# Kernel optimization log

Measured on AMD Instinct MI355X. Metric: run time of the kernel, lower is better.

## Reference

```python
import jax, jax.numpy as jnp
import numpy as np

# Config constants (from cfg in init_kwargs)
B = 4            # batch size (num point clouds)
V = 80000        # total pillars across batch
P = 20           # max points per pillar
C_IN = 4         # x, y, z, intensity
C_OUT = 64       # PillarFeatureNet output channels
NY = NX = 640    # BEV grid
BEV_M = 100.0    # bev_range_m per axis
Z_CUT = 5.0
VX = BEV_M / NX              # 0.15625 m
VY = BEV_M / NY
X_OFF = VX / 2.0 - BEV_M / 2.0   # voxel-center offset, pc_range_min + vx/2
Y_OFF = VY / 2.0 - BEV_M / 2.0
BN_EPS = 1e-3


def setup_inputs() -> dict:
    key = jax.random.key(0)
    k1, k2, k3, k4 = jax.random.split(key, 4)
    # points: xy in [-50, 50), z in [-5, 5), intensity in [0, 1)
    xy = jax.random.uniform(k1, (V, P, 2), jnp.float32, -BEV_M / 2, BEV_M / 2)
    z = jax.random.uniform(k2, (V, P, 1), jnp.float32, -Z_CUT, Z_CUT)
    intensity = jax.random.uniform(k3, (V, P, 1), jnp.float32)
    voxels = jnp.concatenate([xy, z, intensity], axis=-1)  # [V, P, 4]
    num_points = jax.random.randint(k4, (V,), 1, P + 1).astype(jnp.int32)
    # unique pillar coordinates (hard voxelization never emits duplicates)
    rng = np.random.default_rng(0)
    flat = rng.choice(B * NY * NX, size=V, replace=False).astype(np.int32)
    b = flat // (NY * NX)
    rem = flat % (NY * NX)
    y = rem // NX
    x = rem % NX
    coors = jnp.asarray(np.stack([b, np.zeros_like(b), y, x], axis=-1))  # [V,4] (b,z,y,x)
    # PFN layer params: Linear(9->64, bias=False) + BN1d(64)
    W = jax.random.normal(jax.random.fold_in(key, 10), (9, C_OUT), jnp.float32) * 0.05
    gamma = jnp.ones((C_OUT,), jnp.float32)
    beta = jnp.zeros((C_OUT,), jnp.float32)
    running_mean = jnp.zeros((C_OUT,), jnp.float32)
    running_var = jnp.ones((C_OUT,), jnp.float32)
    return {"voxels": voxels, "num_points": num_points, "coors": coors,
            "W": W, "gamma": gamma, "beta": beta,
            "running_mean": running_mean, "running_var": running_var}


def reference(voxels, num_points, coors, W, gamma, beta, running_mean, running_var):
    dt = voxels.dtype
    xyz = voxels[..., :3]                                       # [V,P,3]
    npts = jnp.maximum(num_points, 1).astype(dt)[:, None, None]
    # cluster-center offsets (mean over valid points; padded slots are zero here,
    # matching hard voxelization which zero-pads)
    valid = (jnp.arange(P)[None, :] < num_points[:, None])      # [V,P] bool
    xyz_m = xyz * valid[..., None].astype(dt)
    f_cluster = xyz - jnp.sum(xyz_m, axis=1, keepdims=True) / npts
    # voxel-center offsets (xy only, legacy PillarFeatureNet)
    cx = coors[:, 3].astype(dt)[:, None, None] * VX + X_OFF
    cy = coors[:, 2].astype(dt)[:, None, None] * VY + Y_OFF
    f_center = jnp.concatenate([voxels[..., 0:1] - cx, voxels[..., 1:2] - cy], axis=-1)
    feats = jnp.concatenate([voxels, f_cluster, f_center], axis=-1)  # [V,P,9]
    feats = feats * valid[..., None].astype(dt)
    # PFN layer: linear -> BN1d (eval, running stats) -> relu -> max over points
    h = jnp.einsum('vpi,io->vpo', feats, W)                     # [V,P,64]
    h = (h - running_mean) * jax.lax.rsqrt(running_var + BN_EPS) * gamma + beta
    h = jax.nn.relu(h)
    pillar_feats = jnp.max(h, axis=1)                           # [V,64]
    # scatter to dense BEV canvas [B, C, NY, NX]
    flat = coors[:, 0] * (NY * NX) + coors[:, 2] * NX + coors[:, 3]  # [V]
    canvas = jnp.zeros((B * NY * NX, C_OUT), dt).at[flat].set(pillar_feats)
    canvas = canvas.reshape(B, NY, NX, C_OUT).transpose(0, 3, 1, 2)
    occ = jnp.zeros((B * NY * NX, 1), dt).at[flat].set(jnp.ones((V, 1), dt))
    occ = occ.reshape(B, NY, NX, 1).transpose(0, 3, 1, 2)
    return canvas, occ
```

## Files before the change

kernel.cpp:

```cpp
#include <hip/hip_runtime.h>

constexpr int B_    = 4;
constexpr int V_    = 80000;
constexpr int P_    = 20;
constexpr int COUT  = 64;
constexpr int NX_   = 640;
constexpr int NY_   = 640;
constexpr int NYX   = NX_ * NY_;
constexpr float BEV = 100.0f;
constexpr float VXc = BEV / NX_;
constexpr float VYc = BEV / NY_;
constexpr float XOFF = VXc * 0.5f - BEV * 0.5f;
constexpr float YOFF = VYc * 0.5f - BEV * 0.5f;
constexpr float EPS  = 0.001f;

typedef float  vf4 __attribute__((ext_vector_type(4)));

__global__ __launch_bounds__(256) void pillar_feat_kernel(
    const float* __restrict__ voxels,
    const int*   __restrict__ num_points,
    const int*   __restrict__ coors,
    const float* __restrict__ W,
    const float* __restrict__ gamma_,
    const float* __restrict__ beta_,
    const float* __restrict__ rmean,
    const float* __restrict__ rvar,
    float* __restrict__ feat,
    int*   __restrict__ idxmap)
{
    const int v = blockIdx.x * 4 + (threadIdx.x >> 6);
    const int c = threadIdx.x & 63;
    if (v >= V_) return;

    int n = num_points[v];
    n = n < 1 ? 1 : (n > P_ ? P_ : n);

    const int4 co = ((const int4*)coors)[v];
    const int cb = co.x, cyi = co.z, cxi = co.w;

    const float scale = gamma_[c] * rsqrtf(rvar[c] + EPS);
    const float bias  = beta_[c] - rmean[c] * scale;
    float w[9];
    #pragma unroll
    for (int i = 0; i < 9; ++i) w[i] = W[i * COUT + c] * scale;

    const float wcx = w[0] + w[4] + w[7];
    const float wcy = w[1] + w[5] + w[8];
    const float wcz = w[2] + w[6];
    const float wcw = w[3];

    const float4* __restrict__ pv =
        (const float4*)(voxels + (size_t)v * (P_ * 4));

    float sx = 0.f, sy = 0.f, sz = 0.f;
    float dmax = -3.4e38f;
    for (int p = 0; p < n; ++p) {
        float4 q = pv[p];
        sx += q.x; sy += q.y; sz += q.z;
        float d = q.x * wcx + q.y * wcy + q.z * wcz + q.w * wcw;
        dmax = fmaxf(dmax, d);
    }
    const float inv = 1.0f / (float)n;
    const float ccx = (float)cxi * VXc + XOFF;
    const float ccy = (float)cyi * VYc + YOFF;
    const float btot = bias - (sx * inv) * w[4] - (sy * inv) * w[5]
                            - (sz * inv) * w[6] - ccx * w[7] - ccy * w[8];

    float m = dmax + btot;
    if (n < P_) m = fmaxf(m, bias);

    feat[(size_t)v * COUT + c] = fmaxf(m, 0.0f);

    if (c == 0) idxmap[cb * NYX + cyi * NX_ + cxi] = v;
}

__global__ __launch_bounds__(256) void scatter_kernel(
    const float* __restrict__ feat,
    const int*   __restrict__ idxmap,
    const int*   __restrict__ coors,
    float* __restrict__ canvas,
    float* __restrict__ occ)
{
    const int t = blockIdx.x * blockDim.x + threadIdx.x;
    if (t >= (B_ * NYX) / 4) return;

    int4 id = ((const int4*)idxmap)[t];
    const int cell0 = t * 4;
    const int b   = cell0 / NYX;
    const int rem = cell0 - b * NYX;

    const int4* __restrict__ co4 = (const int4*)coors;
    auto check = [&](int idx, int cell) -> int {
        if (idx < 0 || idx >= V_) return -1;
        int4 co = co4[idx];
        return (co.x * NYX + co.z * NX_ + co.w == cell) ? idx : -1;
    };
    id.x = check(id.x, cell0 + 0);
    id.y = check(id.y, cell0 + 1);
    id.z = check(id.z, cell0 + 2);
    id.w = check(id.w, cell0 + 3);

    vf4 o = { id.x >= 0 ? 1.f : 0.f,
              id.y >= 0 ? 1.f : 0.f,
              id.z >= 0 ? 1.f : 0.f,
              id.w >= 0 ? 1.f : 0.f };
    __builtin_nontemporal_store(o, (vf4*)(occ + cell0));

    const float4* __restrict__ f4 = (const float4*)feat;
    const size_t base = (size_t)b * COUT * NYX + (size_t)rem;

    #pragma unroll
    for (int cg = 0; cg < 16; ++cg) {
        float4 a0 = make_float4(0.f, 0.f, 0.f, 0.f);
        float4 a1 = a0, a2 = a0, a3 = a0;
        if (id.x >= 0) a0 = f4[(size_t)id.x * 16 + cg];
        if (id.y >= 0) a1 = f4[(size_t)id.y * 16 + cg];
        if (id.z >= 0) a2 = f4[(size_t)id.z * 16 + cg];
        if (id.w >= 0) a3 = f4[(size_t)id.w * 16 + cg];
        vf4 s0 = { a0.x, a1.x, a2.x, a3.x };
        vf4 s1 = { a0.y, a1.y, a2.y, a3.y };
        vf4 s2 = { a0.z, a1.z, a2.z, a3.z };
        vf4 s3 = { a0.w, a1.w, a2.w, a3.w };
        float* p0 = canvas + base + (size_t)(4 * cg + 0) * NYX;
        __builtin_nontemporal_store(s0, (vf4*)p0);
        __builtin_nontemporal_store(s1, (vf4*)(p0 + NYX));
        __builtin_nontemporal_store(s2, (vf4*)(p0 + 2 * NYX));
        __builtin_nontemporal_store(s3, (vf4*)(p0 + 3 * NYX));
    }
}

extern "C" void kernel_launch(void* const* d_in, const int* in_sizes, int n_in,
                              void* d_out, int out_size, void* d_ws, size_t ws_size,
                              hipStream_t stream) {
    const float* voxels     = (const float*)d_in[0];
    const int*   num_points = (const int*)  d_in[1];
    const int*   coors      = (const int*)  d_in[2];
    const float* W          = (const float*)d_in[3];
    const float* gamma_     = (const float*)d_in[4];
    const float* beta_      = (const float*)d_in[5];
    const float* rmean      = (const float*)d_in[6];
    const float* rvar       = (const float*)d_in[7];

    float* canvas = (float*)d_out;
    float* occ    = (float*)d_out + (size_t)B_ * COUT * NYX;

    float* feat   = (float*)d_ws;
    int*   idxmap = (int*)((char*)d_ws + (size_t)V_ * COUT * sizeof(float));

    pillar_feat_kernel<<<(V_ + 3) / 4, 256, 0, stream>>>(
        voxels, num_points, coors, W, gamma_, beta_, rmean, rvar, feat, idxmap);

    scatter_kernel<<<(B_ * NYX / 4 + 255) / 256, 256, 0, stream>>>(
        feat, idxmap, coors, canvas, occ);
}
```

Measured before the change: 514.4 us.

## Memset idxmap each call, drop coors validation, unroll point loop

The index map is now cleared to -1 with a memset on every launch. That lets the scatter kernel stop re-reading coors to check whether a stale index matches the cell. Empty cells read from a zeroed row in the workspace, so the loads are no longer predicated. The per-pillar point loop is unrolled by four with masking, which may read past n but stays inside the 20-point pillar. The cost is an extra 6.5 MB memset pass in exchange for fewer dependent gathers in scatter.

```diff
diff --git a/kernel.cpp b/kernel.cpp
--- a/kernel.cpp
+++ b/kernel.cpp
@@ -26,10 +26,14 @@
     const float* __restrict__ rmean,
     const float* __restrict__ rvar,
     float* __restrict__ feat,
-    int*   __restrict__ idxmap)
+    int*   __restrict__ idxmap,
+    float* __restrict__ zrow)
 {
     const int v = blockIdx.x * 4 + (threadIdx.x >> 6);
     const int c = threadIdx.x & 63;
+
+    if (blockIdx.x == 0 && threadIdx.x < COUT) zrow[threadIdx.x] = 0.0f;
+
     if (v >= V_) return;
 
     int n = num_points[v];
@@ -54,11 +58,22 @@
 
     float sx = 0.f, sy = 0.f, sz = 0.f;
     float dmax = -3.4e38f;
-    for (int p = 0; p < n; ++p) {
-        float4 q = pv[p];
-        sx += q.x; sy += q.y; sz += q.z;
-        float d = q.x * wcx + q.y * wcy + q.z * wcz + q.w * wcw;
-        dmax = fmaxf(dmax, d);
+    for (int p0 = 0; p0 < n; p0 += 4) {
+        float4 q0 = pv[p0];
+        float4 q1 = pv[p0 + 1];
+        float4 q2 = pv[p0 + 2];
+        float4 q3 = pv[p0 + 3];
+        #pragma unroll
+        for (int j = 0; j < 4; ++j) {
+            float4 q = (j == 0) ? q0 : (j == 1) ? q1 : (j == 2) ? q2 : q3;
+            const bool ok = (p0 + j) < n;
+            const float msk = ok ? 1.0f : 0.0f;
+            sx = fmaf(q.x, msk, sx);
+            sy = fmaf(q.y, msk, sy);
+            sz = fmaf(q.z, msk, sz);
+            float d = fmaf(q.x, wcx, fmaf(q.y, wcy, fmaf(q.z, wcz, q.w * wcw)));
+            dmax = fmaxf(dmax, ok ? d : -3.4e38f);
+        }
     }
     const float inv = 1.0f / (float)n;
     const float ccx = (float)cxi * VXc + XOFF;
@@ -77,28 +92,25 @@
 __global__ __launch_bounds__(256) void scatter_kernel(
     const float* __restrict__ feat,
     const int*   __restrict__ idxmap,
-    const int*   __restrict__ coors,
+    const float* __restrict__ zrow,
     float* __restrict__ canvas,
     float* __restrict__ occ)
 {
     const int t = blockIdx.x * blockDim.x + threadIdx.x;
     if (t >= (B_ * NYX) / 4) return;
 
-    int4 id = ((const int4*)idxmap)[t];
+    const int4 id = ((const int4*)idxmap)[t];
     const int cell0 = t * 4;
     const int b   = cell0 / NYX;
     const int rem = cell0 - b * NYX;
 
-    const int4* __restrict__ co4 = (const int4*)coors;
-    auto check = [&](int idx, int cell) -> int {
-        if (idx < 0 || idx >= V_) return -1;
-        int4 co = co4[idx];
-        return (co.x * NYX + co.z * NX_ + co.w == cell) ? idx : -1;
-    };
-    id.x = check(id.x, cell0 + 0);
-    id.y = check(id.y, cell0 + 1);
-    id.z = check(id.z, cell0 + 2);
-    id.w = check(id.w, cell0 + 3);
+    const float4* __restrict__ f4 = (const float4*)feat;
+    const float4* __restrict__ z4 = (const float4*)zrow;
+
+    const float4* p0r = (id.x >= 0) ? (f4 + (size_t)id.x * 16) : z4;
+    const float4* p1r = (id.y >= 0) ? (f4 + (size_t)id.y * 16) : z4;
+    const float4* p2r = (id.z >= 0) ? (f4 + (size_t)id.z * 16) : z4;
+    const float4* p3r = (id.w >= 0) ? (f4 + (size_t)id.w * 16) : z4;
 
     vf4 o = { id.x >= 0 ? 1.f : 0.f,
               id.y >= 0 ? 1.f : 0.f,
@@ -106,17 +118,14 @@
               id.w >= 0 ? 1.f : 0.f };
     __builtin_nontemporal_store(o, (vf4*)(occ + cell0));
 
-    const float4* __restrict__ f4 = (const float4*)feat;
     const size_t base = (size_t)b * COUT * NYX + (size_t)rem;
 
     #pragma unroll
     for (int cg = 0; cg < 16; ++cg) {
-        float4 a0 = make_float4(0.f, 0.f, 0.f, 0.f);
-        float4 a1 = a0, a2 = a0, a3 = a0;
-        if (id.x >= 0) a0 = f4[(size_t)id.x * 16 + cg];
-        if (id.y >= 0) a1 = f4[(size_t)id.y * 16 + cg];
-        if (id.z >= 0) a2 = f4[(size_t)id.z * 16 + cg];
-        if (id.w >= 0) a3 = f4[(size_t)id.w * 16 + cg];
+        float4 a0 = p0r[cg];
+        float4 a1 = p1r[cg];
+        float4 a2 = p2r[cg];
+        float4 a3 = p3r[cg];
         vf4 s0 = { a0.x, a1.x, a2.x, a3.x };
         vf4 s1 = { a0.y, a1.y, a2.y, a3.y };
         vf4 s2 = { a0.z, a1.z, a2.z, a3.z };
@@ -146,10 +155,14 @@
 
     float* feat   = (float*)d_ws;
     int*   idxmap = (int*)((char*)d_ws + (size_t)V_ * COUT * sizeof(float));
+    float* zrow   = (float*)((char*)d_ws + (size_t)V_ * COUT * sizeof(float)
+                                         + (size_t)B_ * NYX * sizeof(int));
+
+    hipMemsetAsync(idxmap, 0xFF, (size_t)B_ * NYX * sizeof(int), stream);
 
     pillar_feat_kernel<<<(V_ + 3) / 4, 256, 0, stream>>>(
-        voxels, num_points, coors, W, gamma_, beta_, rmean, rvar, feat, idxmap);
+        voxels, num_points, coors, W, gamma_, beta_, rmean, rvar, feat, idxmap, zrow);
 
     scatter_kernel<<<(B_ * NYX / 4 + 255) / 256, 256, 0, stream>>>(
-        feat, idxmap, coors, canvas, occ);
+        feat, idxmap, zrow, canvas, occ);
 }
```

Measured after the change: 494.1 us. -3.9%, faster.
